# Performance work log

Hardware: AMD Instinct MI355X
Metric: run time of the kernel (lower is better)

The kernel has to match this reference:

```python
import jax, jax.numpy as jnp
import numpy as np

B, S, D = 4, 512, 256
H_SP, W_SP = 64, 64
NUM_HEADS = 8
HEAD_DIM = D // NUM_HEADS


def setup_inputs() -> dict:
    key = jax.random.key(0)
    ks = jax.random.split(key, 10)
    scale = 1.0 / np.sqrt(D)
    return {
        "query": jax.random.normal(ks[0], (B, S, D), dtype=jnp.float32),
        "key_value": jax.random.normal(ks[1], (B, D, H_SP, W_SP), dtype=jnp.float32),
        "Wq": jax.random.normal(ks[2], (D, D), dtype=jnp.float32) * scale,
        "bq": jnp.zeros((D,), dtype=jnp.float32),
        "Wk": jax.random.normal(ks[3], (D, D), dtype=jnp.float32) * scale,
        "bk": jnp.zeros((D,), dtype=jnp.float32),
        "Wv": jax.random.normal(ks[4], (D, D), dtype=jnp.float32) * scale,
        "bv": jnp.zeros((D,), dtype=jnp.float32),
        "Wo": jax.random.normal(ks[5], (D, D), dtype=jnp.float32) * scale,
        "bo": jnp.zeros((D,), dtype=jnp.float32),
    }


def reference(query, key_value, Wq, bq, Wk, bk, Wv, bv, Wo, bo):
    # query: (B, S, D); key_value: (B, D, H, W)
    b, d, h, w = key_value.shape
    s = query.shape[1]
    hw = h * w
    kv = key_value.reshape(b, d, hw).transpose(0, 2, 1)  # (B, HW, D)

    # Linear projections (torch Linear: x @ W.T + b)
    Q = query @ Wq.T + bq                                # (B, S, D)
    K = kv @ Wk.T + bk                                   # (B, HW, D)
    V = kv @ Wv.T + bv                                   # (B, HW, D)

    # Split heads: (B, nH, len, hd)
    Qh = Q.reshape(b, s, NUM_HEADS, HEAD_DIM).transpose(0, 2, 1, 3)
    Kh = K.reshape(b, hw, NUM_HEADS, HEAD_DIM).transpose(0, 2, 1, 3)
    Vh = V.reshape(b, hw, NUM_HEADS, HEAD_DIM).transpose(0, 2, 1, 3)

    scale = HEAD_DIM ** -0.5
    # NOTE: _add_spatial_attention is dead code (returns attn unchanged);
    # norm1/norm2 are never applied in forward; dropout is identity in eval.
    attn = jnp.einsum('bhsd,bhkd->bhsk', Qh, Kh) * scale  # (B, nH, S, HW)
    attn = jax.nn.softmax(attn, axis=-1)
    out = jnp.einsum('bhsk,bhkd->bhsd', attn, Vh)         # (B, nH, S, hd)
    out = out.transpose(0, 2, 1, 3).reshape(b, s, d)      # (B, S, D)
    return out @ Wo.T + bo
```

## Files before the change

### kernel.cpp

```cpp
#include <hip/hip_runtime.h>

constexpr int B_  = 4;
constexpr int S_  = 512;
constexpr int D_  = 256;
constexpr int HW_ = 4096;
constexpr int NH_ = 8;
constexpr int HD_ = 32;
constexpr int NSPLIT = 4;
constexpr int ROWS_  = B_ * NH_ * S_;
constexpr int KVB    = 64;
constexpr int TILES  = HW_ / NSPLIT / KVB;

typedef float  f32x4   __attribute__((ext_vector_type(4)));
typedef float  f32x16  __attribute__((ext_vector_type(16)));
typedef short  s16x4   __attribute__((ext_vector_type(4)));
typedef short  s16x8   __attribute__((ext_vector_type(8)));
typedef __bf16 bf16x8  __attribute__((ext_vector_type(8)));
typedef unsigned int u32x2 __attribute__((ext_vector_type(2)));
typedef unsigned int u32x4 __attribute__((ext_vector_type(4)));

__device__ __forceinline__ f32x4 mfma_bf16(s16x8 a, s16x8 b, f32x4 c) {
  return __builtin_amdgcn_mfma_f32_16x16x32_bf16(
      __builtin_bit_cast(bf16x8, a), __builtin_bit_cast(bf16x8, b), c, 0, 0, 0);
}
__device__ __forceinline__ f32x16 mfma32(s16x8 a, s16x8 b, f32x16 c) {
  return __builtin_amdgcn_mfma_f32_32x32x16_bf16(
      __builtin_bit_cast(bf16x8, a), __builtin_bit_cast(bf16x8, b), c, 0, 0, 0);
}

__device__ __forceinline__ void split4(float4 v, s16x4& h, s16x4& l) {
  float x[4] = {v.x, v.y, v.z, v.w};
  #pragma unroll
  for (int j = 0; j < 4; ++j) {
    unsigned xb = __float_as_uint(x[j]);
    h[j] = (short)(xb >> 16);
    float lo = x[j] - __uint_as_float(xb & 0xFFFF0000u);
    l[j] = (short)((__float_as_uint(lo) + 0x8000u) >> 16);
  }
}

__device__ __forceinline__ unsigned pk_hi(float x, float y) {
  return (__float_as_uint(x) >> 16) | (__float_as_uint(y) & 0xFFFF0000u);
}
__device__ __forceinline__ unsigned pk_lo(float x, float y) {
  float rx = x - __uint_as_float(__float_as_uint(x) & 0xFFFF0000u);
  float ry = y - __uint_as_float(__float_as_uint(y) & 0xFFFF0000u);
  return (__float_as_uint(rx) >> 16) | (__float_as_uint(ry) & 0xFFFF0000u);
}

__global__ __launch_bounds__(256)
void prep(const float* __restrict__ KV,
          short* __restrict__ Th, short* __restrict__ Tl,
          const float* __restrict__ Wk, const float* __restrict__ Wv,
          short* __restrict__ WkH, short* __restrict__ WkL,
          short* __restrict__ WvH, short* __restrict__ WvL,
          const float* __restrict__ query, const float* __restrict__ Wq,
          const float* __restrict__ bq,
          short* __restrict__ Qh, short* __restrict__ Ql, float qalpha)
{
  union SmP {
    struct {
      short Ah[64][40], Al[64][40];
      short W0h[64][40], W0l[64][40];
    } s;
    float ep[64][76];
    float tile[64][65];
  };
  __shared__ __align__(16) SmP sm;
  const int tid = threadIdx.x;
  const int bid0 = blockIdx.x;

  if (bid0 < 1024) {
    const int hwb = bid0 & 63;
    const int db  = (bid0 >> 6) & 3;
    const int b   = bid0 >> 8;
    const int hw0 = hwb * 64, d0 = db * 64;
    #pragma unroll
    for (int i = 0; i < 4; ++i) {
      const int idx = tid + (i << 8);
      const int d = idx >> 4, h4 = idx & 15;
      *(float4*)&sm.tile[d][h4 * 4] =
          *(const float4*)&KV[((size_t)(b * D_ + d0 + d)) * HW_ + hw0 + h4 * 4];
    }
    __syncthreads();
    #pragma unroll
    for (int i = 0; i < 4; ++i) {
      const int idx = tid + (i << 8);
      const int hw = idx >> 4, d4 = idx & 15;
      const float4 v = make_float4(sm.tile[d4*4+0][hw], sm.tile[d4*4+1][hw],
                                   sm.tile[d4*4+2][hw], sm.tile[d4*4+3][hw]);
      s16x4 hh, ll; split4(v, hh, ll);
      const size_t o = ((size_t)(b * HW_ + hw0 + hw)) * D_ + d0 + d4 * 4;
      *(s16x4*)&Th[o] = hh; *(s16x4*)&Tl[o] = ll;
    }
  } else if (bid0 < 1152) {
    const int wv = tid >> 6, lane = tid & 63, lq = lane & 15, lg = lane >> 4;
    const int wm = wv >> 1, wn = wv & 1;
    int bid = bid0 - 1024;
    bid = (bid & 7) * 16 + (bid >> 3);
    const int m0 = (bid & 31) << 6, n0 = (bid >> 5) << 6;

    f32x4 acc0[2][2] = {};
    float4 aF[2], w0R[2];
    auto gload = [&](int kt) {
      const int k0 = kt << 5;
      #pragma unroll
      for (int i = 0; i < 2; ++i) {
        const int idx = tid + (i << 8);
        const int m = idx >> 3, c4 = idx & 7;
        aF[i]  = *(const float4*)&query[(size_t)(m0 + m) * D_ + k0 + c4 * 4];
        w0R[i] = *(const float4*)&Wq[(size_t)(n0 + m) * D_ + k0 + c4 * 4];
      }
    };
    auto stage = [&]() {
      #pragma unroll
      for (int i = 0; i < 2; ++i) {
        const int idx = tid + (i << 8);
        const int m = idx >> 3, c4 = idx & 7;
        s16x4 hh, ll; split4(aF[i], hh, ll);
        *(s16x4*)&sm.s.Ah[m][c4 * 4] = hh;
        *(s16x4*)&sm.s.Al[m][c4 * 4] = ll;
        float4 w = w0R[i];
        w.x *= qalpha; w.y *= qalpha; w.z *= qalpha; w.w *= qalpha;
        split4(w, hh, ll);
        *(s16x4*)&sm.s.W0h[m][c4 * 4] = hh;
        *(s16x4*)&sm.s.W0l[m][c4 * 4] = ll;
      }
    };
    gload(0);
    #pragma unroll
    for (int kt = 0; kt < 8; ++kt) {
      __syncthreads();
      stage();
      __syncthreads();
      if (kt < 7) gload(kt + 1);
      s16x8 ah[2], al[2];
      #pragma unroll
      for (int mi = 0; mi < 2; ++mi) {
        ah[mi] = *(const s16x8*)&sm.s.Ah[wm * 32 + mi * 16 + lq][lg * 8];
        al[mi] = *(const s16x8*)&sm.s.Al[wm * 32 + mi * 16 + lq][lg * 8];
      }
      #pragma unroll
      for (int ni = 0; ni < 2; ++ni) {
        const int nr = wn * 32 + ni * 16 + lq;
        const s16x8 bh = *(const s16x8*)&sm.s.W0h[nr][lg * 8];
        const s16x8 bl = *(const s16x8*)&sm.s.W0l[nr][lg * 8];
        #pragma unroll
        for (int mi = 0; mi < 2; ++mi) {
          acc0[mi][ni] = mfma_bf16(ah[mi], bh, acc0[mi][ni]);
          acc0[mi][ni] = mfma_bf16(al[mi], bh, acc0[mi][ni]);
          acc0[mi][ni] = mfma_bf16(ah[mi], bl, acc0[mi][ni]);
        }
      }
    }
    __syncthreads();
    #pragma unroll
    for (int mi = 0; mi < 2; ++mi)
      #pragma unroll
      for (int ni = 0; ni < 2; ++ni)
        #pragma unroll
        for (int r = 0; r < 4; ++r)
          sm.ep[wm*32 + mi*16 + lg*4 + r][wn*32 + ni*16 + lq] = acc0[mi][ni][r];
    __syncthreads();
    #pragma unroll
    for (int i = 0; i < 4; ++i) {
      const int idx = tid + (i << 8);
      const int m = idx >> 4, c4 = idx & 15;
      const float4 v = *(const float4*)&sm.ep[m][c4 * 4];
      const float4 bb = *(const float4*)&bq[n0 + c4 * 4];
      const float4 o = make_float4(v.x + qalpha * bb.x, v.y + qalpha * bb.y,
                                   v.z + qalpha * bb.z, v.w + qalpha * bb.w);
      s16x4 hh, ll; split4(o, hh, ll);
      const size_t off = (size_t)(m0 + m) * D_ + n0 + c4 * 4;
      *(s16x4*)&Qh[off] = hh;
      *(s16x4*)&Ql[off] = ll;
    }
  } else {
    const int idx = (bid0 - 1152) * 256 + tid;
    const int m = idx >> 14;
    const int o4 = idx & 16383;
    const float4 v = *(const float4*)&(m ? Wv : Wk)[o4 * 4];
    s16x4 hh, ll; split4(v, hh, ll);
    *(s16x4*)&(m ? WvH : WkH)[o4 * 4] = hh;
    *(s16x4*)&(m ? WvL : WkL)[o4 * 4] = ll;
  }
}

__global__ __launch_bounds__(256)
void gemm_kv(const short* __restrict__ Ah_, const short* __restrict__ Al_,
             const short* __restrict__ W0h_, const short* __restrict__ W0l_,
             const float* __restrict__ b0,
             short* __restrict__ C0h, short* __restrict__ C0l,
             const short* __restrict__ W1h_, const short* __restrict__ W1l_,
             const float* __restrict__ b1,
             short* __restrict__ C1h, short* __restrict__ C1l)
{
  union Sm {
    struct {
      short Ah[64][40], Al[64][40];
      short W0h[64][40], W0l[64][40];
      short W1h[64][40], W1l[64][40];
    } s;
    float ep[64][76];
  };
  __shared__ __align__(16) Sm sm;

  const int tid = threadIdx.x;
  const int wv = tid >> 6, lane = tid & 63, lq = lane & 15, lg = lane >> 4;
  const int wm = wv >> 1, wn = wv & 1;
  constexpr int nx = (B_ * HW_) >> 6;
  int bid = blockIdx.x;
  bid = (bid & 7) * 128 + (bid >> 3);
  const int m0 = (bid % nx) << 6, n0 = (bid / nx) << 6;

  f32x4 acc0[2][2] = {};
  f32x4 acc1[2][2] = {};
  s16x8 aH, aL, w0H, w0L, w1H, w1L;

  const int mq = tid >> 2, c8 = tid & 3;
  auto gload = [&](int kt) {
    const int k0 = kt << 5;
    const size_t aoff = (size_t)(m0 + mq) * D_ + k0 + c8 * 8;
    aH = *(const s16x8*)&Ah_[aoff];
    aL = *(const s16x8*)&Al_[aoff];
    const size_t woff = (size_t)(n0 + mq) * D_ + k0 + c8 * 8;
    w0H = *(const s16x8*)&W0h_[woff];
    w0L = *(const s16x8*)&W0l_[woff];
    w1H = *(const s16x8*)&W1h_[woff];
    w1L = *(const s16x8*)&W1l_[woff];
  };
  auto stage = [&]() {
    *(s16x8*)&sm.s.Ah[mq][c8 * 8]  = aH;
    *(s16x8*)&sm.s.Al[mq][c8 * 8]  = aL;
    *(s16x8*)&sm.s.W0h[mq][c8 * 8] = w0H;
    *(s16x8*)&sm.s.W0l[mq][c8 * 8] = w0L;
    *(s16x8*)&sm.s.W1h[mq][c8 * 8] = w1H;
    *(s16x8*)&sm.s.W1l[mq][c8 * 8] = w1L;
  };

  gload(0);
  #pragma unroll
  for (int kt = 0; kt < 8; ++kt) {
    __syncthreads();
    stage();
    __syncthreads();
    if (kt < 7) gload(kt + 1);
    s16x8 ah[2], al[2];
    #pragma unroll
    for (int mi = 0; mi < 2; ++mi) {
      ah[mi] = *(const s16x8*)&sm.s.Ah[wm * 32 + mi * 16 + lq][lg * 8];
      al[mi] = *(const s16x8*)&sm.s.Al[wm * 32 + mi * 16 + lq][lg * 8];
    }
    #pragma unroll
    for (int ni = 0; ni < 2; ++ni) {
      const int nr = wn * 32 + ni * 16 + lq;
      const s16x8 bh = *(const s16x8*)&sm.s.W0h[nr][lg * 8];
      const s16x8 bl = *(const s16x8*)&sm.s.W0l[nr][lg * 8];
      #pragma unroll
      for (int mi = 0; mi < 2; ++mi) {
        acc0[mi][ni] = mfma_bf16(ah[mi], bh, acc0[mi][ni]);
        acc0[mi][ni] = mfma_bf16(al[mi], bh, acc0[mi][ni]);
        acc0[mi][ni] = mfma_bf16(ah[mi], bl, acc0[mi][ni]);
      }
      const s16x8 ch = *(const s16x8*)&sm.s.W1h[nr][lg * 8];
      const s16x8 cl = *(const s16x8*)&sm.s.W1l[nr][lg * 8];
      #pragma unroll
      for (int mi = 0; mi < 2; ++mi) {
        acc1[mi][ni] = mfma_bf16(ah[mi], ch, acc1[mi][ni]);
        acc1[mi][ni] = mfma_bf16(al[mi], ch, acc1[mi][ni]);
        acc1[mi][ni] = mfma_bf16(ah[mi], cl, acc1[mi][ni]);
      }
    }
  }

  __syncthreads();
  #pragma unroll
  for (int mi = 0; mi < 2; ++mi)
    #pragma unroll
    for (int ni = 0; ni < 2; ++ni)
      #pragma unroll
      for (int r = 0; r < 4; ++r)
        sm.ep[wm*32 + mi*16 + lg*4 + r][wn*32 + ni*16 + lq] = acc0[mi][ni][r];
  __syncthreads();
  #pragma unroll
  for (int i = 0; i < 4; ++i) {
    const int idx = tid + (i << 8);
    const int m = idx >> 4, c4 = idx & 15;
    const float4 v = *(const float4*)&sm.ep[m][c4 * 4];
    const float4 bb = *(const float4*)&b0[n0 + c4 * 4];
    const float4 o = make_float4(v.x + bb.x, v.y + bb.y, v.z + bb.z, v.w + bb.w);
    const size_t off = (size_t)(m0 + m) * D_ + n0 + c4 * 4;
    s16x4 hh, ll; split4(o, hh, ll);
    *(s16x4*)&C0h[off] = hh;
    *(s16x4*)&C0l[off] = ll;
  }

  __syncthreads();
  #pragma unroll
  for (int mi = 0; mi < 2; ++mi)
    #pragma unroll
    for (int ni = 0; ni < 2; ++ni)
      *(f32x4*)&sm.ep[wn*32 + ni*16 + lq][wm*32 + mi*16 + lg*4] = acc1[mi][ni];
  __syncthreads();
  const int b = m0 >> 12, hw0 = m0 & (HW_ - 1);
  #pragma unroll
  for (int i = 0; i < 4; ++i) {
    const int idx = tid + (i << 8);
    const int n = idx >> 4, m4 = idx & 15;
    const float4 v = *(const float4*)&sm.ep[n][m4 * 4];
    const float bb = b1[n0 + n];
    const float4 o = make_float4(v.x + bb, v.y + bb, v.z + bb, v.w + bb);
    s16x4 hh, ll; split4(o, hh, ll);
    const size_t off = ((size_t)(b * D_ + n0 + n)) * HW_ + hw0 + m4 * 4;
    *(s16x4*)&C1h[off] = hh;
    *(s16x4*)&C1l[off] = ll;
  }
}

__global__ __launch_bounds__(256, 4)
void attn_mfma32(const short* __restrict__ Qh_, const short* __restrict__ Ql_,
                 const short* __restrict__ Kh_, const short* __restrict__ Kl_,
                 const short* __restrict__ Vth, const short* __restrict__ Vtl,
                 float* __restrict__ Opart, float* __restrict__ Ml)
{
  union Sm {
    short V[2][2][32][72];
    float ep[4][32][33];
  };
  __shared__ __align__(16) Sm sm;

  const int tid  = threadIdx.x;
  const int wv   = tid >> 6, lane = tid & 63;
  const int lq   = lane & 31, hi = lane >> 5;

  int w = blockIdx.x;
  w = (w & 7) * 64 + (w >> 3);
  const int qt = w & 3;
  const int h  = (w >> 2) & 7;
  const int b  = (w >> 5) & 3;
  const int sp = w >> 7;
  const int q0 = qt * 128 + wv * 32;

  s16x8 qh[2], ql[2];
  {
    const size_t qb = ((size_t)(b * S_ + q0 + lq)) * D_ + h * HD_ + hi * 8;
    qh[0] = *(const s16x8*)&Qh_[qb];      qh[1] = *(const s16x8*)&Qh_[qb + 16];
    ql[0] = *(const s16x8*)&Ql_[qb];      ql[1] = *(const s16x8*)&Ql_[qb + 16];
  }

  f32x16 o = {0.f,0.f,0.f,0.f, 0.f,0.f,0.f,0.f, 0.f,0.f,0.f,0.f, 0.f,0.f,0.f,0.f};
  float lrun = 0.f;

  const int dd = tid >> 3, c8 = tid & 7;
  s16x8 vrH, vrL;
  auto gloadV = [&](int t) {
    const size_t a = ((size_t)(b * D_ + h * HD_ + dd)) * HW_ + (size_t)t * KVB + c8 * 8;
    vrH = *(const s16x8*)&Vth[a];
    vrL = *(const s16x8*)&Vtl[a];
  };
  auto writeV = [&](int p) {
    *(s16x8*)&sm.V[p][0][dd][c8 * 8] = vrH;
    *(s16x8*)&sm.V[p][1][dd][c8 * 8] = vrL;
  };

  int p = 0;
  gloadV(sp * TILES);
  writeV(0);

  for (int tt = 0; tt < TILES; ++tt) {
    const int t = sp * TILES + tt;
    if (tt + 1 < TILES) gloadV(t + 1);
    __syncthreads();

    f32x16 sc[2];
    #pragma unroll
    for (int cc = 0; cc < 2; ++cc) {
      const size_t kb = ((size_t)(b * HW_ + t * KVB + cc * 32 + lq)) * D_ + h * HD_ + hi * 8;
      const s16x8 kh0 = *(const s16x8*)&Kh_[kb];
      const s16x8 kh1 = *(const s16x8*)&Kh_[kb + 16];
      const s16x8 kl0 = *(const s16x8*)&Kl_[kb];
      const s16x8 kl1 = *(const s16x8*)&Kl_[kb + 16];
      f32x16 a = {0.f,0.f,0.f,0.f, 0.f,0.f,0.f,0.f, 0.f,0.f,0.f,0.f, 0.f,0.f,0.f,0.f};
      __builtin_amdgcn_s_setprio(1);
      a = mfma32(kh0, qh[0], a);
      a = mfma32(kh1, qh[1], a);
      a = mfma32(kl0, qh[0], a);
      a = mfma32(kl1, qh[1], a);
      a = mfma32(kh0, ql[0], a);
      a = mfma32(kh1, ql[1], a);
      __builtin_amdgcn_s_setprio(0);
      sc[cc] = a;
    }

    #pragma unroll
    for (int cc = 0; cc < 2; ++cc)
      #pragma unroll
      for (int r = 0; r < 16; ++r) sc[cc][r] = exp2f(sc[cc][r]);
    float tr[16];
    #pragma unroll
    for (int r = 0; r < 16; ++r) tr[r] = sc[0][r] + sc[1][r];
    #pragma unroll
    for (int s = 8; s > 0; s >>= 1)
      #pragma unroll
      for (int r = 0; r < s; ++r) tr[r] += tr[r + s];
    lrun += tr[0];

    #pragma unroll
    for (int wn = 0; wn < 4; ++wn) {
      const int cc = wn >> 1, base = (wn & 1) * 8;
      const unsigned a_h = pk_hi(sc[cc][base+0], sc[cc][base+1]);
      const unsigned b_h = pk_hi(sc[cc][base+4], sc[cc][base+5]);
      const unsigned c_h = pk_hi(sc[cc][base+2], sc[cc][base+3]);
      const unsigned d_h = pk_hi(sc[cc][base+6], sc[cc][base+7]);
      const unsigned a_l = pk_lo(sc[cc][base+0], sc[cc][base+1]);
      const unsigned b_l = pk_lo(sc[cc][base+4], sc[cc][base+5]);
      const unsigned c_l = pk_lo(sc[cc][base+2], sc[cc][base+3]);
      const unsigned d_l = pk_lo(sc[cc][base+6], sc[cc][base+7]);
      const u32x2 s1 = __builtin_amdgcn_permlane32_swap(a_h, b_h, false, false);
      const u32x2 s2 = __builtin_amdgcn_permlane32_swap(c_h, d_h, false, false);
      const u32x2 s3 = __builtin_amdgcn_permlane32_swap(a_l, b_l, false, false);
      const u32x2 s4 = __builtin_amdgcn_permlane32_swap(c_l, d_l, false, false);
      const u32x4 wH = {s1[0], s2[0], s1[1], s2[1]};
      const u32x4 wL = {s3[0], s4[0], s3[1], s4[1]};
      const s16x8 pH = __builtin_bit_cast(s16x8, wH);
      const s16x8 pL = __builtin_bit_cast(s16x8, wL);
      const s16x8 vh = *(const s16x8*)&sm.V[p][0][lq][wn * 16 + hi * 8];
      const s16x8 vl = *(const s16x8*)&sm.V[p][1][lq][wn * 16 + hi * 8];
      __builtin_amdgcn_s_setprio(1);
      o = mfma32(vh, pH, o);
      o = mfma32(vl, pH, o);
      o = mfma32(vh, pL, o);
      __builtin_amdgcn_s_setprio(0);
    }

    if (tt + 1 < TILES) writeV(p ^ 1);
    p ^= 1;
  }

  lrun += __shfl_xor(lrun, 32);
  __syncthreads();
  if (lane < 32) {
    const int g = (b * NH_ + h) * S_ + q0 + lq;
    Ml[(size_t)sp * ROWS_ + g] = lrun;
  }
  #pragma unroll
  for (int r = 0; r < 16; ++r) {
    const int d = (r & 3) + 8 * (r >> 2) + 4 * hi;
    sm.ep[wv][lq][d] = o[r];
  }
  const int qq = lane >> 1, d0 = (lane & 1) * 16;
  const int g2 = (b * NH_ + h) * S_ + q0 + qq;
  float* dst = &Opart[((size_t)sp * ROWS_ + g2) * HD_ + d0];
  #pragma unroll
  for (int j = 0; j < 4; ++j)
    *(float4*)(dst + j * 4) = *(const float4*)&sm.ep[wv][qq][d0 + j * 4];
}

__global__ __launch_bounds__(256)
void oproj(const float* __restrict__ Opart, const float* __restrict__ Ml,
           const float* __restrict__ Wo, const float* __restrict__ bo,
           float* __restrict__ out)
{
  union Sm {
    struct {
      short Ah[64][40], Al[64][40];
      short W0h[64][40], W0l[64][40];
    } s;
    float ep[64][76];
  };
  __shared__ __align__(16) Sm sm;

  const int tid = threadIdx.x;
  const int wv = tid >> 6, lane = tid & 63, lq = lane & 15, lg = lane >> 4;
  const int wm = wv >> 1, wn = wv & 1;
  int bid = blockIdx.x;
  bid = (bid & 7) * 16 + (bid >> 3);
  const int m0 = (bid & 31) << 6, n0 = (bid >> 5) << 6;

  f32x4 acc0[2][2] = {};

  const int ar = tid >> 2, dc = (tid & 3) * 8;
  const int ab = (m0 + ar) >> 9, aq = (m0 + ar) & (S_ - 1);
  float4 oR[8];
  float lsum;
  float4 w0R[2];

  auto gload = [&](int kt) {
    const int g = (ab * NH_ + kt) * S_ + aq;
    float ls = 0.f;
    #pragma unroll
    for (int s = 0; s < NSPLIT; ++s) ls += Ml[(size_t)s * ROWS_ + g];
    lsum = ls;
    #pragma unroll
    for (int s = 0; s < NSPLIT; ++s) {
      const size_t base = ((size_t)s * ROWS_ + g) * HD_ + dc;
      oR[s * 2 + 0] = *(const float4*)&Opart[base];
      oR[s * 2 + 1] = *(const float4*)&Opart[base + 4];
    }
    const int k0 = kt << 5;
    #pragma unroll
    for (int i = 0; i < 2; ++i) {
      const int idx = tid + (i << 8);
      const int n = idx >> 3, c4 = idx & 7;
      w0R[i] = *(const float4*)&Wo[(size_t)(n0 + n) * D_ + k0 + c4 * 4];
    }
  };
  auto stage = [&]() {
    const float inv = 1.0f / lsum;
    float4 a0 = make_float4(
        (oR[0].x + oR[2].x + oR[4].x + oR[6].x) * inv,
        (oR[0].y + oR[2].y + oR[4].y + oR[6].y) * inv,
        (oR[0].z + oR[2].z + oR[4].z + oR[6].z) * inv,
        (oR[0].w + oR[2].w + oR[4].w + oR[6].w) * inv);
    float4 a1 = make_float4(
        (oR[1].x + oR[3].x + oR[5].x + oR[7].x) * inv,
        (oR[1].y + oR[3].y + oR[5].y + oR[7].y) * inv,
        (oR[1].z + oR[3].z + oR[5].z + oR[7].z) * inv,
        (oR[1].w + oR[3].w + oR[5].w + oR[7].w) * inv);
    s16x4 hh, ll;
    split4(a0, hh, ll);
    *(s16x4*)&sm.s.Ah[ar][dc]     = hh;
    *(s16x4*)&sm.s.Al[ar][dc]     = ll;
    split4(a1, hh, ll);
    *(s16x4*)&sm.s.Ah[ar][dc + 4] = hh;
    *(s16x4*)&sm.s.Al[ar][dc + 4] = ll;
    #pragma unroll
    for (int i = 0; i < 2; ++i) {
      const int idx = tid + (i << 8);
      const int n = idx >> 3, c4 = idx & 7;
      s16x4 wh, wl; split4(w0R[i], wh, wl);
      *(s16x4*)&sm.s.W0h[n][c4 * 4] = wh;
      *(s16x4*)&sm.s.W0l[n][c4 * 4] = wl;
    }
  };

  gload(0);
  #pragma unroll
  for (int kt = 0; kt < 8; ++kt) {
    __syncthreads();
    stage();
    __syncthreads();
    if (kt < 7) gload(kt + 1);
    s16x8 ah[2], al[2];
    #pragma unroll
    for (int mi = 0; mi < 2; ++mi) {
      ah[mi] = *(const s16x8*)&sm.s.Ah[wm * 32 + mi * 16 + lq][lg * 8];
      al[mi] = *(const s16x8*)&sm.s.Al[wm * 32 + mi * 16 + lq][lg * 8];
    }
    #pragma unroll
    for (int ni = 0; ni < 2; ++ni) {
      const int nr = wn * 32 + ni * 16 + lq;
      const s16x8 bh = *(const s16x8*)&sm.s.W0h[nr][lg * 8];
      const s16x8 bl = *(const s16x8*)&sm.s.W0l[nr][lg * 8];
      #pragma unroll
      for (int mi = 0; mi < 2; ++mi) {
        acc0[mi][ni] = mfma_bf16(ah[mi], bh, acc0[mi][ni]);
        acc0[mi][ni] = mfma_bf16(al[mi], bh, acc0[mi][ni]);
        acc0[mi][ni] = mfma_bf16(ah[mi], bl, acc0[mi][ni]);
      }
    }
  }

  __syncthreads();
  #pragma unroll
  for (int mi = 0; mi < 2; ++mi)
    #pragma unroll
    for (int ni = 0; ni < 2; ++ni)
      #pragma unroll
      for (int r = 0; r < 4; ++r)
        sm.ep[wm*32 + mi*16 + lg*4 + r][wn*32 + ni*16 + lq] = acc0[mi][ni][r];
  __syncthreads();
  #pragma unroll
  for (int i = 0; i < 4; ++i) {
    const int idx = tid + (i << 8);
    const int m = idx >> 4, c4 = idx & 15;
    const float4 v = *(const float4*)&sm.ep[m][c4 * 4];
    const float4 bb = *(const float4*)&bo[n0 + c4 * 4];
    *(float4*)&out[(size_t)(m0 + m) * D_ + n0 + c4 * 4] =
        make_float4(v.x + bb.x, v.y + bb.y, v.z + bb.z, v.w + bb.w);
  }
}

extern "C" void kernel_launch(void* const* d_in, const int* in_sizes, int n_in,
                              void* d_out, int out_size, void* d_ws, size_t ws_size,
                              hipStream_t stream)
{
  const float* query = (const float*)d_in[0];
  const float* keyva = (const float*)d_in[1];
  const float* Wq = (const float*)d_in[2];
  const float* bq = (const float*)d_in[3];
  const float* Wk = (const float*)d_in[4];
  const float* bk = (const float*)d_in[5];
  const float* Wv = (const float*)d_in[6];
  const float* bv = (const float*)d_in[7];
  const float* Wo = (const float*)d_in[8];
  const float* bo = (const float*)d_in[9];
  float* out = (float*)d_out;

  char* w = (char*)d_ws;
  short* KvtH = (short*)w; w += 8388608;
  short* KvtL = (short*)w; w += 8388608;
  short* Qh   = (short*)w; w += 1048576;
  short* Ql   = (short*)w; w += 1048576;
  short* Kh   = (short*)w; w += 8388608;
  short* Kl   = (short*)w; w += 8388608;
  short* VtH  = (short*)w; w += 8388608;
  short* VtL  = (short*)w; w += 8388608;
  short* WkH  = (short*)w; w += 262144;
  short* WkL  = (short*)w; w += 262144;
  short* WvH  = (short*)w; w += 262144;
  short* WvL  = (short*)w; w += 262144;
  float* Ml   = (float*)w; w += 262144;
  float* Opart= (float*)KvtH;

  const dim3 blk(256);
  const float qscale = 0.17677669529663687f * 1.4426950408889634f;

  prep<<<dim3(1280), blk, 0, stream>>>(
      keyva, KvtH, KvtL, Wk, Wv, WkH, WkL, WvH, WvL,
      query, Wq, bq, Qh, Ql, qscale);

  gemm_kv<<<dim3(1024), blk, 0, stream>>>(
      KvtH, KvtL, WkH, WkL, bk, Kh, Kl, WvH, WvL, bv, VtH, VtL);

  attn_mfma32<<<dim3(NSPLIT * B_ * NH_ * (S_ / 128)), blk, 0, stream>>>(
      Qh, Ql, Kh, Kl, VtH, VtL, Opart, Ml);

  oproj<<<dim3(128), blk, 0, stream>>>(Opart, Ml, Wo, bo, out);
}
```

Measured before the change: 172.3 us.

## Drop LDS staging in KV GEMM and attention, double KV split count

The K/V projection GEMM and the attention kernel now read operands straight from global memory into MFMA registers instead of staging them through shared memory with barriers. The attention kernel also fuses exp and PV accumulation per 32-key chunk to lower register pressure. The KV split factor goes from 4 to 8 to launch more attention blocks, with the Ml buffer sized to match and occupancy hints lowered. The output projection now sums the partial results inside its load loop. The intent is to remove LDS round-trips and barrier stalls and to fill more CUs. The cost is more redundant global/L2 traffic, since each wave fetches its own tiles, plus a larger partial-output buffer for the reduction to read.

```diff
diff --git a/kernel.cpp b/kernel.cpp
--- a/kernel.cpp
+++ b/kernel.cpp
@@ -6,7 +6,7 @@
 constexpr int HW_ = 4096;
 constexpr int NH_ = 8;
 constexpr int HD_ = 32;
-constexpr int NSPLIT = 4;
+constexpr int NSPLIT = 8;
 constexpr int ROWS_  = B_ * NH_ * S_;
 constexpr int KVB    = 64;
 constexpr int TILES  = HW_ / NSPLIT / KVB;
@@ -195,15 +195,7 @@
              const float* __restrict__ b1,
              short* __restrict__ C1h, short* __restrict__ C1l)
 {
-  union Sm {
-    struct {
-      short Ah[64][40], Al[64][40];
-      short W0h[64][40], W0l[64][40];
-      short W1h[64][40], W1l[64][40];
-    } s;
-    float ep[64][76];
-  };
-  __shared__ __align__(16) Sm sm;
+  __shared__ __align__(16) float ep[64][76];
 
   const int tid = threadIdx.x;
   const int wv = tid >> 6, lane = tid & 63, lq = lane & 15, lg = lane >> 4;
@@ -215,55 +207,33 @@
 
   f32x4 acc0[2][2] = {};
   f32x4 acc1[2][2] = {};
-  s16x8 aH, aL, w0H, w0L, w1H, w1L;
-
-  const int mq = tid >> 2, c8 = tid & 3;
-  auto gload = [&](int kt) {
-    const int k0 = kt << 5;
-    const size_t aoff = (size_t)(m0 + mq) * D_ + k0 + c8 * 8;
-    aH = *(const s16x8*)&Ah_[aoff];
-    aL = *(const s16x8*)&Al_[aoff];
-    const size_t woff = (size_t)(n0 + mq) * D_ + k0 + c8 * 8;
-    w0H = *(const s16x8*)&W0h_[woff];
-    w0L = *(const s16x8*)&W0l_[woff];
-    w1H = *(const s16x8*)&W1h_[woff];
-    w1L = *(const s16x8*)&W1l_[woff];
-  };
-  auto stage = [&]() {
-    *(s16x8*)&sm.s.Ah[mq][c8 * 8]  = aH;
-    *(s16x8*)&sm.s.Al[mq][c8 * 8]  = aL;
-    *(s16x8*)&sm.s.W0h[mq][c8 * 8] = w0H;
-    *(s16x8*)&sm.s.W0l[mq][c8 * 8] = w0L;
-    *(s16x8*)&sm.s.W1h[mq][c8 * 8] = w1H;
-    *(s16x8*)&sm.s.W1l[mq][c8 * 8] = w1L;
-  };
-
-  gload(0);
+
+  const size_t arow[2] = {(size_t)(m0 + wm * 32 + lq) * D_,
+                          (size_t)(m0 + wm * 32 + 16 + lq) * D_};
+  const size_t wrow[2] = {(size_t)(n0 + wn * 32 + lq) * D_,
+                          (size_t)(n0 + wn * 32 + 16 + lq) * D_};
+
   #pragma unroll
   for (int kt = 0; kt < 8; ++kt) {
-    __syncthreads();
-    stage();
-    __syncthreads();
-    if (kt < 7) gload(kt + 1);
+    const int k0 = kt * 32 + lg * 8;
     s16x8 ah[2], al[2];
     #pragma unroll
     for (int mi = 0; mi < 2; ++mi) {
-      ah[mi] = *(const s16x8*)&sm.s.Ah[wm * 32 + mi * 16 + lq][lg * 8];
-      al[mi] = *(const s16x8*)&sm.s.Al[wm * 32 + mi * 16 + lq][lg * 8];
+      ah[mi] = *(const s16x8*)&Ah_[arow[mi] + k0];
+      al[mi] = *(const s16x8*)&Al_[arow[mi] + k0];
     }
     #pragma unroll
     for (int ni = 0; ni < 2; ++ni) {
-      const int nr = wn * 32 + ni * 16 + lq;
-      const s16x8 bh = *(const s16x8*)&sm.s.W0h[nr][lg * 8];
-      const s16x8 bl = *(const s16x8*)&sm.s.W0l[nr][lg * 8];
+      const s16x8 bh = *(const s16x8*)&W0h_[wrow[ni] + k0];
+      const s16x8 bl = *(const s16x8*)&W0l_[wrow[ni] + k0];
       #pragma unroll
       for (int mi = 0; mi < 2; ++mi) {
         acc0[mi][ni] = mfma_bf16(ah[mi], bh, acc0[mi][ni]);
         acc0[mi][ni] = mfma_bf16(al[mi], bh, acc0[mi][ni]);
         acc0[mi][ni] = mfma_bf16(ah[mi], bl, acc0[mi][ni]);
       }
-      const s16x8 ch = *(const s16x8*)&sm.s.W1h[nr][lg * 8];
-      const s16x8 cl = *(const s16x8*)&sm.s.W1l[nr][lg * 8];
+      const s16x8 ch = *(const s16x8*)&W1h_[wrow[ni] + k0];
+      const s16x8 cl = *(const s16x8*)&W1l_[wrow[ni] + k0];
       #pragma unroll
       for (int mi = 0; mi < 2; ++mi) {
         acc1[mi][ni] = mfma_bf16(ah[mi], ch, acc1[mi][ni]);
@@ -273,20 +243,19 @@
     }
   }
 
-  __syncthreads();
   #pragma unroll
   for (int mi = 0; mi < 2; ++mi)
     #pragma unroll
     for (int ni = 0; ni < 2; ++ni)
       #pragma unroll
       for (int r = 0; r < 4; ++r)
-        sm.ep[wm*32 + mi*16 + lg*4 + r][wn*32 + ni*16 + lq] = acc0[mi][ni][r];
+        ep[wm*32 + mi*16 + lg*4 + r][wn*32 + ni*16 + lq] = acc0[mi][ni][r];
   __syncthreads();
   #pragma unroll
   for (int i = 0; i < 4; ++i) {
     const int idx = tid + (i << 8);
     const int m = idx >> 4, c4 = idx & 15;
-    const float4 v = *(const float4*)&sm.ep[m][c4 * 4];
+    const float4 v = *(const float4*)&ep[m][c4 * 4];
     const float4 bb = *(const float4*)&b0[n0 + c4 * 4];
     const float4 o = make_float4(v.x + bb.x, v.y + bb.y, v.z + bb.z, v.w + bb.w);
     const size_t off = (size_t)(m0 + m) * D_ + n0 + c4 * 4;
@@ -300,14 +269,14 @@
   for (int mi = 0; mi < 2; ++mi)
     #pragma unroll
     for (int ni = 0; ni < 2; ++ni)
-      *(f32x4*)&sm.ep[wn*32 + ni*16 + lq][wm*32 + mi*16 + lg*4] = acc1[mi][ni];
+      *(f32x4*)&ep[wn*32 + ni*16 + lq][wm*32 + mi*16 + lg*4] = acc1[mi][ni];
   __syncthreads();
   const int b = m0 >> 12, hw0 = m0 & (HW_ - 1);
   #pragma unroll
   for (int i = 0; i < 4; ++i) {
     const int idx = tid + (i << 8);
     const int n = idx >> 4, m4 = idx & 15;
-    const float4 v = *(const float4*)&sm.ep[n][m4 * 4];
+    const float4 v = *(const float4*)&ep[n][m4 * 4];
     const float bb = b1[n0 + n];
     const float4 o = make_float4(v.x + bb, v.y + bb, v.z + bb, v.w + bb);
     s16x4 hh, ll; split4(o, hh, ll);
@@ -317,24 +286,20 @@
   }
 }
 
-__global__ __launch_bounds__(256, 4)
+__global__ __launch_bounds__(256, 3)
 void attn_mfma32(const short* __restrict__ Qh_, const short* __restrict__ Ql_,
                  const short* __restrict__ Kh_, const short* __restrict__ Kl_,
                  const short* __restrict__ Vth, const short* __restrict__ Vtl,
                  float* __restrict__ Opart, float* __restrict__ Ml)
 {
-  union Sm {
-    short V[2][2][32][72];
-    float ep[4][32][33];
-  };
-  __shared__ __align__(16) Sm sm;
+  __shared__ __align__(16) float ep[4][32][33];
 
   const int tid  = threadIdx.x;
   const int wv   = tid >> 6, lane = tid & 63;
   const int lq   = lane & 31, hi = lane >> 5;
 
   int w = blockIdx.x;
-  w = (w & 7) * 64 + (w >> 3);
+  w = (w & 7) * 128 + (w >> 3);
   const int qt = w & 3;
   const int h  = (w >> 2) & 7;
   const int b  = (w >> 5) & 3;
@@ -351,28 +316,10 @@
   f32x16 o = {0.f,0.f,0.f,0.f, 0.f,0.f,0.f,0.f, 0.f,0.f,0.f,0.f, 0.f,0.f,0.f,0.f};
   float lrun = 0.f;
 
-  const int dd = tid >> 3, c8 = tid & 7;
-  s16x8 vrH, vrL;
-  auto gloadV = [&](int t) {
-    const size_t a = ((size_t)(b * D_ + h * HD_ + dd)) * HW_ + (size_t)t * KVB + c8 * 8;
-    vrH = *(const s16x8*)&Vth[a];
-    vrL = *(const s16x8*)&Vtl[a];
-  };
-  auto writeV = [&](int p) {
-    *(s16x8*)&sm.V[p][0][dd][c8 * 8] = vrH;
-    *(s16x8*)&sm.V[p][1][dd][c8 * 8] = vrL;
-  };
-
-  int p = 0;
-  gloadV(sp * TILES);
-  writeV(0);
+  const size_t vrow = ((size_t)(b * D_ + h * HD_ + lq)) * HW_;
 
   for (int tt = 0; tt < TILES; ++tt) {
     const int t = sp * TILES + tt;
-    if (tt + 1 < TILES) gloadV(t + 1);
-    __syncthreads();
-
-    f32x16 sc[2];
     #pragma unroll
     for (int cc = 0; cc < 2; ++cc) {
       const size_t kb = ((size_t)(b * HW_ + t * KVB + cc * 32 + lq)) * D_ + h * HD_ + hi * 8;
@@ -389,56 +336,50 @@
       a = mfma32(kh0, ql[0], a);
       a = mfma32(kh1, ql[1], a);
       __builtin_amdgcn_s_setprio(0);
-      sc[cc] = a;
-    }
-
-    #pragma unroll
-    for (int cc = 0; cc < 2; ++cc)
-      #pragma unroll
-      for (int r = 0; r < 16; ++r) sc[cc][r] = exp2f(sc[cc][r]);
-    float tr[16];
-    #pragma unroll
-    for (int r = 0; r < 16; ++r) tr[r] = sc[0][r] + sc[1][r];
-    #pragma unroll
-    for (int s = 8; s > 0; s >>= 1)
-      #pragma unroll
-      for (int r = 0; r < s; ++r) tr[r] += tr[r + s];
-    lrun += tr[0];
-
-    #pragma unroll
-    for (int wn = 0; wn < 4; ++wn) {
-      const int cc = wn >> 1, base = (wn & 1) * 8;
-      const unsigned a_h = pk_hi(sc[cc][base+0], sc[cc][base+1]);
-      const unsigned b_h = pk_hi(sc[cc][base+4], sc[cc][base+5]);
-      const unsigned c_h = pk_hi(sc[cc][base+2], sc[cc][base+3]);
-      const unsigned d_h = pk_hi(sc[cc][base+6], sc[cc][base+7]);
-      const unsigned a_l = pk_lo(sc[cc][base+0], sc[cc][base+1]);
-      const unsigned b_l = pk_lo(sc[cc][base+4], sc[cc][base+5]);
-      const unsigned c_l = pk_lo(sc[cc][base+2], sc[cc][base+3]);
-      const unsigned d_l = pk_lo(sc[cc][base+6], sc[cc][base+7]);
-      const u32x2 s1 = __builtin_amdgcn_permlane32_swap(a_h, b_h, false, false);
-      const u32x2 s2 = __builtin_amdgcn_permlane32_swap(c_h, d_h, false, false);
-      const u32x2 s3 = __builtin_amdgcn_permlane32_swap(a_l, b_l, false, false);
-      const u32x2 s4 = __builtin_amdgcn_permlane32_swap(c_l, d_l, false, false);
-      const u32x4 wH = {s1[0], s2[0], s1[1], s2[1]};
-      const u32x4 wL = {s3[0], s4[0], s3[1], s4[1]};
-      const s16x8 pH = __builtin_bit_cast(s16x8, wH);
-      const s16x8 pL = __builtin_bit_cast(s16x8, wL);
-      const s16x8 vh = *(const s16x8*)&sm.V[p][0][lq][wn * 16 + hi * 8];
-      const s16x8 vl = *(const s16x8*)&sm.V[p][1][lq][wn * 16 + hi * 8];
-      __builtin_amdgcn_s_setprio(1);
-      o = mfma32(vh, pH, o);
-      o = mfma32(vl, pH, o);
-      o = mfma32(vh, pL, o);
-      __builtin_amdgcn_s_setprio(0);
-    }
-
-    if (tt + 1 < TILES) writeV(p ^ 1);
-    p ^= 1;
+
+      #pragma unroll
+      for (int r = 0; r < 16; ++r) a[r] = exp2f(a[r]);
+      float tr[8];
+      #pragma unroll
+      for (int r = 0; r < 8; ++r) tr[r] = a[r] + a[r + 8];
+      #pragma unroll
+      for (int s = 4; s > 0; s >>= 1)
+        #pragma unroll
+        for (int r = 0; r < s; ++r) tr[r] += tr[r + s];
+      lrun += tr[0];
+
+      #pragma unroll
+      for (int j = 0; j < 2; ++j) {
+        const int base = j * 8;
+        const unsigned a_h = pk_hi(a[base+0], a[base+1]);
+        const unsigned b_h = pk_hi(a[base+4], a[base+5]);
+        const unsigned c_h = pk_hi(a[base+2], a[base+3]);
+        const unsigned d_h = pk_hi(a[base+6], a[base+7]);
+        const unsigned a_l = pk_lo(a[base+0], a[base+1]);
+        const unsigned b_l = pk_lo(a[base+4], a[base+5]);
+        const unsigned c_l = pk_lo(a[base+2], a[base+3]);
+        const unsigned d_l = pk_lo(a[base+6], a[base+7]);
+        const u32x2 s1 = __builtin_amdgcn_permlane32_swap(a_h, b_h, false, false);
+        const u32x2 s2 = __builtin_amdgcn_permlane32_swap(c_h, d_h, false, false);
+        const u32x2 s3 = __builtin_amdgcn_permlane32_swap(a_l, b_l, false, false);
+        const u32x2 s4 = __builtin_amdgcn_permlane32_swap(c_l, d_l, false, false);
+        const u32x4 wH = {s1[0], s2[0], s1[1], s2[1]};
+        const u32x4 wL = {s3[0], s4[0], s3[1], s4[1]};
+        const s16x8 pH = __builtin_bit_cast(s16x8, wH);
+        const s16x8 pL = __builtin_bit_cast(s16x8, wL);
+        const size_t vb = vrow + (size_t)t * KVB + (cc * 2 + j) * 16 + hi * 8;
+        const s16x8 vh = *(const s16x8*)&Vth[vb];
+        const s16x8 vl = *(const s16x8*)&Vtl[vb];
+        __builtin_amdgcn_s_setprio(1);
+        o = mfma32(vh, pH, o);
+        o = mfma32(vl, pH, o);
+        o = mfma32(vh, pL, o);
+        __builtin_amdgcn_s_setprio(0);
+      }
+    }
   }
 
   lrun += __shfl_xor(lrun, 32);
-  __syncthreads();
   if (lane < 32) {
     const int g = (b * NH_ + h) * S_ + q0 + lq;
     Ml[(size_t)sp * ROWS_ + g] = lrun;
@@ -446,14 +387,14 @@
   #pragma unroll
   for (int r = 0; r < 16; ++r) {
     const int d = (r & 3) + 8 * (r >> 2) + 4 * hi;
-    sm.ep[wv][lq][d] = o[r];
+    ep[wv][lq][d] = o[r];
   }
   const int qq = lane >> 1, d0 = (lane & 1) * 16;
   const int g2 = (b * NH_ + h) * S_ + q0 + qq;
   float* dst = &Opart[((size_t)sp * ROWS_ + g2) * HD_ + d0];
   #pragma unroll
   for (int j = 0; j < 4; ++j)
-    *(float4*)(dst + j * 4) = *(const float4*)&sm.ep[wv][qq][d0 + j * 4];
+    *(float4*)(dst + j * 4) = *(const float4*)&ep[wv][qq][d0 + j * 4];
 }
 
 __global__ __launch_bounds__(256)
@@ -481,22 +422,25 @@
 
   const int ar = tid >> 2, dc = (tid & 3) * 8;
   const int ab = (m0 + ar) >> 9, aq = (m0 + ar) & (S_ - 1);
-  float4 oR[8];
+  float4 a0s, a1s;
   float lsum;
   float4 w0R[2];
 
   auto gload = [&](int kt) {
     const int g = (ab * NH_ + kt) * S_ + aq;
     float ls = 0.f;
-    #pragma unroll
-    for (int s = 0; s < NSPLIT; ++s) ls += Ml[(size_t)s * ROWS_ + g];
-    lsum = ls;
+    float4 s0 = make_float4(0.f, 0.f, 0.f, 0.f);
+    float4 s1 = make_float4(0.f, 0.f, 0.f, 0.f);
     #pragma unroll
     for (int s = 0; s < NSPLIT; ++s) {
+      ls += Ml[(size_t)s * ROWS_ + g];
       const size_t base = ((size_t)s * ROWS_ + g) * HD_ + dc;
-      oR[s * 2 + 0] = *(const float4*)&Opart[base];
-      oR[s * 2 + 1] = *(const float4*)&Opart[base + 4];
-    }
+      const float4 o0 = *(const float4*)&Opart[base];
+      const float4 o1 = *(const float4*)&Opart[base + 4];
+      s0.x += o0.x; s0.y += o0.y; s0.z += o0.z; s0.w += o0.w;
+      s1.x += o1.x; s1.y += o1.y; s1.z += o1.z; s1.w += o1.w;
+    }
+    lsum = ls; a0s = s0; a1s = s1;
     const int k0 = kt << 5;
     #pragma unroll
     for (int i = 0; i < 2; ++i) {
@@ -507,16 +451,8 @@
   };
   auto stage = [&]() {
     const float inv = 1.0f / lsum;
-    float4 a0 = make_float4(
-        (oR[0].x + oR[2].x + oR[4].x + oR[6].x) * inv,
-        (oR[0].y + oR[2].y + oR[4].y + oR[6].y) * inv,
-        (oR[0].z + oR[2].z + oR[4].z + oR[6].z) * inv,
-        (oR[0].w + oR[2].w + oR[4].w + oR[6].w) * inv);
-    float4 a1 = make_float4(
-        (oR[1].x + oR[3].x + oR[5].x + oR[7].x) * inv,
-        (oR[1].y + oR[3].y + oR[5].y + oR[7].y) * inv,
-        (oR[1].z + oR[3].z + oR[5].z + oR[7].z) * inv,
-        (oR[1].w + oR[3].w + oR[5].w + oR[7].w) * inv);
+    float4 a0 = make_float4(a0s.x * inv, a0s.y * inv, a0s.z * inv, a0s.w * inv);
+    float4 a1 = make_float4(a1s.x * inv, a1s.y * inv, a1s.z * inv, a1s.w * inv);
     s16x4 hh, ll;
     split4(a0, hh, ll);
     *(s16x4*)&sm.s.Ah[ar][dc]     = hh;
@@ -610,7 +546,7 @@
   short* WkL  = (short*)w; w += 262144;
   short* WvH  = (short*)w; w += 262144;
   short* WvL  = (short*)w; w += 262144;
-  float* Ml   = (float*)w; w += 262144;
+  float* Ml   = (float*)w; w += 524288;
   float* Opart= (float*)KvtH;
 
   const dim3 blk(256);
```

After: 224.4 us. 30.3% more time.
